# Optimization experiments

Hardware: AMD Instinct MI355X
Metric: run time of the kernel (lower is better)

Reference implementation:

```python
import jax, jax.numpy as jnp
import numpy as np

MAX_LEN = 2048  # config.max_len; T == MAX_LEN here
NEG_FILL = float(np.iinfo(np.int32).min)  # exact masked-fill constant from source


def sinusoidal_pe(max_len, d_feature):
    # sinusoidal_init(max_len=2*config.max_len, squeeze=True) from the source
    pe = np.zeros((max_len, d_feature), dtype=np.float32)
    position = np.arange(0, max_len)[:, np.newaxis]
    scale_factor = -np.log(10000.0 / 1.0) / (d_feature // 2 - 1)
    div_term = 1.0 * np.exp(np.arange(0, d_feature // 2) * scale_factor)
    pe[:, :d_feature // 2] = np.sin(position * div_term)
    pe[:, d_feature // 2:2 * (d_feature // 2)] = np.cos(position * div_term)
    return jnp.asarray(pe)


def rel_shift_causal(logits):
    # logits: [B, T, T] (square -> causal branch of relative_shift), batched version
    b, t1, t2 = logits.shape
    pad = jnp.zeros_like(logits[..., :1])
    x = jnp.concatenate((pad, logits), axis=-1)      # [B, T, T+1]
    x = jnp.reshape(x, (b, t2 + 1, t1))
    x = x[:, 1:, :]                                  # drop first row
    return jnp.reshape(x, (b, t1, t2))


def setup_inputs() -> dict:
    key = jax.random.key(0)
    ks = jax.random.split(key, 7)
    B, T, D = 8, 2048, 512
    s = 1.0 / np.sqrt(D)
    inputs = jax.random.normal(ks[0], (B, T, D), dtype=jnp.float32)
    Wq = jax.random.normal(ks[1], (D, D), dtype=jnp.float32) * s
    Wk = jax.random.normal(ks[2], (D, D), dtype=jnp.float32) * s
    Wv = jax.random.normal(ks[3], (D, D), dtype=jnp.float32) * s
    Wrel = jax.random.normal(ks[4], (D, D), dtype=jnp.float32) * s
    content_bias = jax.random.normal(ks[5], (D,), dtype=jnp.float32) * 0.02
    relative_bias = jax.random.normal(ks[6], (D,), dtype=jnp.float32) * 0.02
    # causal mask as built by nn.make_causal_mask: [B, 1, T, T]
    mask = jnp.tril(jnp.ones((T, T), dtype=bool))[None, None].repeat(B, axis=0)
    return {"inputs": inputs, "Wq": Wq, "Wk": Wk, "Wv": Wv, "Wrel": Wrel,
            "content_bias": content_bias, "relative_bias": relative_bias, "mask": mask}


def reference(inputs, Wq, Wk, Wv, Wrel, content_bias, relative_bias, mask):
    B, T, D = inputs.shape
    q = inputs @ Wq
    k = inputs @ Wk
    v = inputs @ Wv
    # content attention with learned content bias
    content_att = jnp.einsum('bqd,bkd->bqk', q + content_bias, k)
    # relative position attention (causal, idxs=None): pe slice [mid-T : mid]
    pe = sinusoidal_pe(2 * MAX_LEN, D)[MAX_LEN - T:MAX_LEN]  # [T, D]
    relative_key = pe @ Wrel                                  # Dense(no bias)
    relative_att = jnp.einsum('bqd,kd->bqk', q + relative_bias, relative_key)
    relative_att = rel_shift_causal(relative_att)
    attn = (content_att + relative_att) / jnp.sqrt(jnp.asarray(D, inputs.dtype))
    attn = jnp.where(mask.squeeze(1), attn, NEG_FILL)
    attn = jax.nn.softmax(attn, axis=-1)
    return attn @ v
```

## Files before the change

kernel.cpp:

```cpp
#include <hip/hip_runtime.h>

typedef __attribute__((ext_vector_type(8))) short short8;
typedef __attribute__((ext_vector_type(4))) float f32x4;
typedef __attribute__((ext_vector_type(4))) float fvec4;
typedef __attribute__((ext_vector_type(4))) unsigned short us4;

#define T_ 2048
#define D_ 512
#define SC_ 0.04419417382415922f

__device__ __forceinline__ unsigned short f2bf(float f) {
    unsigned int u = __float_as_uint(f);
    u += 0x7fffu + ((u >> 16) & 1u);
    return (unsigned short)(u >> 16);
}

__device__ __forceinline__ void gload16(const void* g, void* l) {
    __builtin_amdgcn_global_load_lds((const __attribute__((address_space(1))) unsigned int*)g,
                                     (__attribute__((address_space(3))) unsigned int*)l,
                                     16, 0, 0);
}

__global__ __launch_bounds__(256) void prep_all(
    const float* __restrict__ in_f,
    const float* __restrict__ Wq, const float* __restrict__ Wk,
    const float* __restrict__ Wv, const float* __restrict__ Wr,
    unsigned short* __restrict__ in_bf,
    unsigned short* __restrict__ WqT, unsigned short* __restrict__ WkT,
    unsigned short* __restrict__ WvT, unsigned short* __restrict__ WrT,
    unsigned short* __restrict__ pe)
{
    const int bb = blockIdx.x;
    const int tid = threadIdx.x;
    if (bb < 8192) {
        const int idx = bb * 256 + tid;
        fvec4 v = ((const fvec4*)in_f)[idx];
        us4 o;
        o.x = f2bf(v.x); o.y = f2bf(v.y); o.z = f2bf(v.z); o.w = f2bf(v.w);
        ((us4*)in_bf)[idx] = o;
    } else if (bb < 9216) {
        __shared__ float wt[32][33];
        const int t = bb - 8192;
        const int w = t >> 8, tile = t & 255;
        const int tr = (tile >> 4) * 32, tc = (tile & 15) * 32;
        const float* W = (w == 0) ? Wq : (w == 1) ? Wk : (w == 2) ? Wv : Wr;
        unsigned short* WT = (w == 0) ? WqT : (w == 1) ? WkT : (w == 2) ? WvT : WrT;
        const int r0 = tid >> 5, c0 = tid & 31;
#pragma unroll
        for (int p = 0; p < 4; ++p)
            wt[r0 + 8 * p][c0] = W[(long)(tr + r0 + 8 * p) * 512 + tc + c0];
        __syncthreads();
#pragma unroll
        for (int p = 0; p < 4; ++p)
            WT[(long)(tc + r0 + 8 * p) * 512 + tr + c0] = f2bf(wt[c0][r0 + 8 * p]);
    } else {
        const int idx = (bb - 9216) * 256 + tid;
        const int o = idx * 4;
        const int rpos = o >> 9;
        us4 ov;
#pragma unroll
        for (int e = 0; e < 4; ++e) {
            const int c = (o + e) & 511;
            const int ci = (c < 256) ? c : c - 256;
            const float dv = expf((float)ci * -0.03611898183128701f);
            const float ang = (float)rpos * dv;
            ((unsigned short*)&ov)[e] = f2bf((c < 256) ? sinf(ang) : cosf(ang));
        }
        ((us4*)pe)[idx] = ov;
    }
}

struct __align__(16) SMem {
    unsigned short At[128 * 64];
    unsigned short Bt[128 * 64];
};

__device__ __forceinline__ void gemm_core(const unsigned short* __restrict__ A, long lda,
                                          const unsigned short* __restrict__ B, long ldb,
                                          int kmax, SMem& sm, f32x4 (&acc)[4][4]) {
    const int tid = threadIdx.x;
    const int wid = tid >> 6;
    const int lane = tid & 63;
    const int quad = lane >> 4;
    const int lr = lane & 15;
    const int wm = (wid & 1) * 64;
    const int wn = (wid >> 1) * 64;
#pragma unroll
    for (int r = 0; r < 4; ++r)
#pragma unroll
        for (int c = 0; c < 4; ++c) acc[r][c] = (f32x4){0.f, 0.f, 0.f, 0.f};

    const int sr = tid >> 3;
    const int l8 = ((tid & 7) ^ (sr & 7)) * 8;
    const unsigned short* Ag = A + (long)sr * lda + l8;
    const unsigned short* Bg = B + (long)sr * ldb + l8;

    for (int kk = 0; kk < kmax; kk += 64) {
#pragma unroll
        for (int c = 0; c < 4; ++c) {
            gload16(Ag + (long)(32 * c) * lda + kk, &sm.At[c * 2048 + wid * 512]);
            gload16(Bg + (long)(32 * c) * ldb + kk, &sm.Bt[c * 2048 + wid * 512]);
        }
        __syncthreads();
#pragma unroll
        for (int ks = 0; ks < 2; ++ks) {
            short8 av[4], bv[4];
#pragma unroll
            for (int r = 0; r < 4; ++r) {
                const int row = wm + r * 16 + lr;
                av[r] = *(const short8*)&sm.At[row * 64 + (((ks * 4 + quad) ^ (row & 7)) * 8)];
            }
#pragma unroll
            for (int c = 0; c < 4; ++c) {
                const int row = wn + c * 16 + lr;
                bv[c] = *(const short8*)&sm.Bt[row * 64 + (((ks * 4 + quad) ^ (row & 7)) * 8)];
            }
#pragma unroll
            for (int r = 0; r < 4; ++r)
#pragma unroll
                for (int c = 0; c < 4; ++c)
                    acc[r][c] = __builtin_amdgcn_mfma_f32_16x16x32_bf16(av[r], bv[c], acc[r][c], 0, 0, 0);
        }
        __syncthreads();
    }
}

#define EPI_COORDS()                               \
    const int tid = threadIdx.x;                   \
    const int wid = tid >> 6;                      \
    const int lane = tid & 63;                     \
    const int quad = lane >> 4;                    \
    const int lr = lane & 15;                      \
    const int wm = (wid & 1) * 64;                 \
    const int wn = (wid >> 1) * 64;

__global__ __launch_bounds__(256, 3) void proj_kernel(
    const unsigned short* __restrict__ in_bf,
    const unsigned short* __restrict__ WqT, const unsigned short* __restrict__ WkT,
    const unsigned short* __restrict__ WvT, const unsigned short* __restrict__ WrT,
    const unsigned short* __restrict__ pe,
    const float* __restrict__ cb, const float* __restrict__ rb,
    unsigned short* __restrict__ qc, unsigned short* __restrict__ qr,
    unsigned short* __restrict__ kbf, unsigned short* __restrict__ vT,
    unsigned short* __restrict__ rk)
{
    __shared__ SMem sm;
    EPI_COORDS();
    const long TD = (long)T_ * D_;
    const long DT = (long)D_ * T_;
    f32x4 acc[4][4];
    const int t = blockIdx.x;
    if (t < 1024) {
        const int r = t & 511;
        const int it = r >> 2, jt = r & 3;
        const unsigned short* Bw = (t < 512) ? WqT : WkT;
        gemm_core(in_bf + (long)it * 128 * 512, 512, Bw + (long)jt * 128 * 512, 512, 512, sm, acc);
        const int i0 = it * 128, j0 = jt * 128;
#pragma unroll
        for (int r2 = 0; r2 < 4; ++r2)
#pragma unroll
            for (int c2 = 0; c2 < 4; ++c2) {
                const int gi = i0 + wm + r2 * 16 + quad * 4;
                const int gj = j0 + wn + c2 * 16 + lr;
#pragma unroll
                for (int tt = 0; tt < 4; ++tt) {
                    const float v = acc[r2][c2][tt];
                    const long row = gi + tt;
                    if (t < 512) {
                        qc[row * 512 + gj] = f2bf(v + cb[gj]);
                        qr[row * 512 + gj] = f2bf(v + rb[gj]);
                    } else {
                        kbf[row * 512 + gj] = f2bf(v);
                    }
                }
            }
    } else if (t < 1536) {
        const int r = t - 1024;
        const int z = r >> 6, rr = r & 63;
        const int it = rr >> 4, jt = rr & 15;
        const int i0 = it * 128, j0 = jt * 128;
        gemm_core(WvT + (long)i0 * 512, 512, in_bf + (long)z * TD + (long)j0 * 512, 512, 512, sm, acc);
#pragma unroll
        for (int r2 = 0; r2 < 4; ++r2)
#pragma unroll
            for (int c2 = 0; c2 < 4; ++c2) {
                const int gi = i0 + wm + r2 * 16 + quad * 4;
                const int gj = j0 + wn + c2 * 16 + lr;
#pragma unroll
                for (int tt = 0; tt < 4; ++tt)
                    vT[(long)z * DT + (long)(gi + tt) * 2048 + gj] = f2bf(acc[r2][c2][tt]);
            }
    } else {
        const int r = t - 1536;
        const int it = r >> 2, jt = r & 3;
        const int i0 = it * 128, j0 = jt * 128;
        gemm_core(pe + (long)i0 * 512, 512, WrT + (long)j0 * 512, 512, 512, sm, acc);
#pragma unroll
        for (int r2 = 0; r2 < 4; ++r2)
#pragma unroll
            for (int c2 = 0; c2 < 4; ++c2) {
                const int gi = i0 + wm + r2 * 16 + quad * 4;
                const int gj = j0 + wn + c2 * 16 + lr;
#pragma unroll
                for (int tt = 0; tt < 4; ++tt)
                    rk[(long)(gi + tt) * 512 + gj] = f2bf(acc[r2][c2][tt]);
            }
    }
}

__global__ __launch_bounds__(256, 3) void score_kernel(
    const unsigned short* __restrict__ qc, const unsigned short* __restrict__ qr,
    const unsigned short* __restrict__ kbf, const unsigned short* __restrict__ rk,
    float* __restrict__ C8, float* __restrict__ R8)
{
    __shared__ SMem sm;
    EPI_COORDS();
    const long TD = (long)T_ * D_;
    f32x4 acc[4][4];
    const int z = blockIdx.x & 7;
    const int rr = blockIdx.x >> 3;
    if (rr < 136) {
        const int r = rr;
        int a = (int)((sqrtf(8.f * (float)r + 1.f) - 1.f) * 0.5f);
        if ((a + 1) * (a + 2) / 2 <= r) ++a;
        if (a * (a + 1) / 2 > r) --a;
        const int b = r - a * (a + 1) / 2;
        const int i0 = a * 128, j0 = b * 128;
        gemm_core(qc + (long)z * TD + (long)i0 * 512, 512,
                  kbf + (long)z * TD + (long)j0 * 512, 512, 512, sm, acc);
        float* Cf = C8 + (long)z * 4194304L;
#pragma unroll
        for (int r2 = 0; r2 < 4; ++r2)
#pragma unroll
            for (int c2 = 0; c2 < 4; ++c2) {
                const int gi = i0 + wm + r2 * 16 + quad * 4;
                const int gj = j0 + wn + c2 * 16 + lr;
#pragma unroll
                for (int tt = 0; tt < 4; ++tt)
                    Cf[(long)(gi + tt) * 2048 + gj] = acc[r2][c2][tt] * SC_;
            }
    } else {
        const int r = rr - 136;
        int u = (int)((sqrtf(8.f * (float)r + 1.f) - 1.f) * 0.5f);
        if ((u + 1) * (u + 2) / 2 <= r) ++u;
        if (u * (u + 1) / 2 > r) --u;
        const int v2 = r - u * (u + 1) / 2;
        const int a = u, b = 15 - u + v2;
        const int i0 = a * 128, p0 = b * 128;
        gemm_core(qr + (long)z * TD + (long)i0 * 512, 512,
                  rk + (long)p0 * 512, 512, 512, sm, acc);
        float* Rf = R8 + (long)z * 4194304L;
#pragma unroll
        for (int r2 = 0; r2 < 4; ++r2)
#pragma unroll
            for (int c2 = 0; c2 < 4; ++c2) {
                const int gi = i0 + wm + r2 * 16 + quad * 4;
                const int gp = p0 + wn + c2 * 16 + lr;
#pragma unroll
                for (int tt = 0; tt < 4; ++tt)
                    Rf[(long)(gi + tt) * 2048 + gp] = acc[r2][c2][tt];
            }
    }
}

__global__ __launch_bounds__(256) void softmax_kernel(float* __restrict__ C8,
                                                      const float* __restrict__ R8) {
    float* Cm = C8 + (long)blockIdx.y * 4194304L;
    const float* Rm = R8 + (long)blockIdx.y * 4194304L;
    __shared__ float s[2048];
    __shared__ float red[8];
    const int tid = threadIdx.x;
    const int wid = tid >> 6;
    for (int ss = 0; ss < 8; ++ss) {
        const int i = blockIdx.x + 256 * ss;
        const int n = i + 1;
        float* crow = Cm + (long)i * 2048;
        const float* rrow = Rm + (long)i * 2048 + (2047 - i);
        __syncthreads();
        float lmax = -3.0e38f;
        for (int j = tid; j < n; j += 256) {
            float v = crow[j] + rrow[j] * SC_;
            s[j] = v; lmax = fmaxf(lmax, v);
        }
        for (int o = 32; o; o >>= 1) lmax = fmaxf(lmax, __shfl_down(lmax, o));
        if ((tid & 63) == 0) red[wid] = lmax;
        __syncthreads();
        if (tid == 0) red[4] = fmaxf(fmaxf(red[0], red[1]), fmaxf(red[2], red[3]));
        __syncthreads();
        const float m = red[4];
        float lsum = 0.f;
        for (int j = tid; j < n; j += 256) { float e = __expf(s[j] - m); s[j] = e; lsum += e; }
        for (int o = 32; o; o >>= 1) lsum += __shfl_down(lsum, o);
        __syncthreads();
        if ((tid & 63) == 0) red[wid] = lsum;
        __syncthreads();
        if (tid == 0) red[4] = 1.0f / (red[0] + red[1] + red[2] + red[3]);
        __syncthreads();
        const float inv = red[4];
        unsigned short* P = (unsigned short*)Cm;
        const int iend = ((i >> 7) + 1) << 7;
        for (int j = tid; j < iend; j += 256) {
            const float pv = (j < n) ? s[j] * inv : 0.f;
            P[(long)i * 4096 + j] = f2bf(pv);
        }
    }
}

__global__ __launch_bounds__(256, 3) void pv_kernel(
    const float* __restrict__ C8, const unsigned short* __restrict__ vT,
    float* __restrict__ out)
{
    __shared__ SMem sm;
    EPI_COORDS();
    const long TD = (long)T_ * D_;
    const long DT = (long)D_ * T_;
    f32x4 acc[4][4];
    const int z = blockIdx.x & 7;
    const int q = blockIdx.x >> 3;
    const int it = 15 - (q >> 2);
    const int jt = q & 3;
    const int i0 = it * 128, j0 = jt * 128;
    const int kmax = i0 + 128;
    gemm_core((const unsigned short*)(C8 + (long)z * 4194304L) + (long)i0 * 4096, 4096,
              vT + (long)z * DT + (long)j0 * 2048, 2048, kmax, sm, acc);
#pragma unroll
    for (int r2 = 0; r2 < 4; ++r2)
#pragma unroll
        for (int c2 = 0; c2 < 4; ++c2) {
            const int gi = i0 + wm + r2 * 16 + quad * 4;
            const int gj = j0 + wn + c2 * 16 + lr;
#pragma unroll
            for (int tt = 0; tt < 4; ++tt)
                out[(long)z * TD + (long)(gi + tt) * 512 + gj] = acc[r2][c2][tt];
        }
}

extern "C" void kernel_launch(void* const* d_in, const int* in_sizes, int n_in,
                              void* d_out, int out_size, void* d_ws, size_t ws_size,
                              hipStream_t stream) {
    (void)in_sizes; (void)n_in; (void)out_size; (void)ws_size;
    const float* inputs = (const float*)d_in[0];
    const float* Wq = (const float*)d_in[1];
    const float* Wk = (const float*)d_in[2];
    const float* Wv = (const float*)d_in[3];
    const float* Wrel = (const float*)d_in[4];
    const float* cb = (const float*)d_in[5];
    const float* rb = (const float*)d_in[6];
    float* out = (float*)d_out;

    char* ws = (char*)d_ws;
    unsigned short* in_bf = (unsigned short*)ws;
    unsigned short* WqT = (unsigned short*)(ws + 16777216);
    unsigned short* WkT = WqT + 262144;
    unsigned short* WvT = WkT + 262144;
    unsigned short* WrT = WvT + 262144;
    unsigned short* pe  = WrT + 262144;
    unsigned short* qc  = pe + 1048576;
    unsigned short* qr  = qc + 8388608;
    unsigned short* kbf = qr + 8388608;
    unsigned short* vT  = kbf + 8388608;
    unsigned short* rk  = vT + 8388608;
    float* C8 = (float*)(rk + 1048576);
    float* R8 = C8 + 33554432;

    prep_all<<<dim3(10240), 256, 0, stream>>>(inputs, Wq, Wk, Wv, Wrel,
                                              in_bf, WqT, WkT, WvT, WrT, pe);
    proj_kernel<<<dim3(1600), 256, 0, stream>>>(in_bf, WqT, WkT, WvT, WrT, pe, cb, rb,
                                                qc, qr, kbf, vT, rk);
    score_kernel<<<dim3(2176), 256, 0, stream>>>(qc, qr, kbf, rk, C8, R8);
    softmax_kernel<<<dim3(256, 8), 256, 0, stream>>>(C8, R8);
    pv_kernel<<<dim3(512), 256, 0, stream>>>(C8, vT, out);
}
```

Baseline: 375.9 us.

## Pre-shift and pre-scale relative scores in GEMM epilogue, vectorize softmax

```diff
diff --git a/kernel.cpp b/kernel.cpp
--- a/kernel.cpp
+++ b/kernel.cpp
@@ -257,52 +257,78 @@
                 const int gi = i0 + wm + r2 * 16 + quad * 4;
                 const int gp = p0 + wn + c2 * 16 + lr;
 #pragma unroll
-                for (int tt = 0; tt < 4; ++tt)
-                    Rf[(long)(gi + tt) * 2048 + gp] = acc[r2][c2][tt];
+                for (int tt = 0; tt < 4; ++tt) {
+                    const int row = gi + tt;
+                    const int j = gp + row - 2047;
+                    if (j >= 0)
+                        Rf[(long)row * 2048 + j] = acc[r2][c2][tt] * SC_;
+                }
             }
     }
 }
 
 __global__ __launch_bounds__(256) void softmax_kernel(float* __restrict__ C8,
                                                       const float* __restrict__ R8) {
+    const int i = blockIdx.x;
     float* Cm = C8 + (long)blockIdx.y * 4194304L;
     const float* Rm = R8 + (long)blockIdx.y * 4194304L;
     __shared__ float s[2048];
-    __shared__ float red[8];
+    __shared__ float red[5];
     const int tid = threadIdx.x;
     const int wid = tid >> 6;
-    for (int ss = 0; ss < 8; ++ss) {
-        const int i = blockIdx.x + 256 * ss;
-        const int n = i + 1;
-        float* crow = Cm + (long)i * 2048;
-        const float* rrow = Rm + (long)i * 2048 + (2047 - i);
-        __syncthreads();
-        float lmax = -3.0e38f;
-        for (int j = tid; j < n; j += 256) {
-            float v = crow[j] + rrow[j] * SC_;
-            s[j] = v; lmax = fmaxf(lmax, v);
-        }
-        for (int o = 32; o; o >>= 1) lmax = fmaxf(lmax, __shfl_down(lmax, o));
-        if ((tid & 63) == 0) red[wid] = lmax;
-        __syncthreads();
-        if (tid == 0) red[4] = fmaxf(fmaxf(red[0], red[1]), fmaxf(red[2], red[3]));
-        __syncthreads();
-        const float m = red[4];
-        float lsum = 0.f;
-        for (int j = tid; j < n; j += 256) { float e = __expf(s[j] - m); s[j] = e; lsum += e; }
-        for (int o = 32; o; o >>= 1) lsum += __shfl_down(lsum, o);
-        __syncthreads();
-        if ((tid & 63) == 0) red[wid] = lsum;
-        __syncthreads();
-        if (tid == 0) red[4] = 1.0f / (red[0] + red[1] + red[2] + red[3]);
-        __syncthreads();
-        const float inv = red[4];
-        unsigned short* P = (unsigned short*)Cm;
-        const int iend = ((i >> 7) + 1) << 7;
-        for (int j = tid; j < iend; j += 256) {
+    const int n = i + 1;
+    const int n4 = (n + 3) >> 2;
+    const f32x4* c4 = (const f32x4*)(Cm + (long)i * 2048);
+    const f32x4* r4 = (const f32x4*)(Rm + (long)i * 2048);
+    float lmax = -3.0e38f;
+    for (int j4 = tid; j4 < n4; j4 += 256) {
+        const f32x4 c = c4[j4];
+        const f32x4 r = r4[j4];
+        f32x4 v;
+#pragma unroll
+        for (int e = 0; e < 4; ++e) {
+            const int j = j4 * 4 + e;
+            const float vv = (j < n) ? c[e] + r[e] : -3.0e38f;
+            v[e] = vv;
+            lmax = fmaxf(lmax, vv);
+        }
+        *(f32x4*)&s[j4 * 4] = v;
+    }
+    for (int o = 32; o; o >>= 1) lmax = fmaxf(lmax, __shfl_down(lmax, o));
+    if ((tid & 63) == 0) red[wid] = lmax;
+    __syncthreads();
+    if (tid == 0) red[4] = fmaxf(fmaxf(red[0], red[1]), fmaxf(red[2], red[3]));
+    __syncthreads();
+    const float m = red[4];
+    float lsum = 0.f;
+    for (int j4 = tid; j4 < n4; j4 += 256) {
+        f32x4 v = *(f32x4*)&s[j4 * 4];
+#pragma unroll
+        for (int e = 0; e < 4; ++e) {
+            const float x = __expf(v[e] - m);
+            v[e] = x;
+            lsum += x;
+        }
+        *(f32x4*)&s[j4 * 4] = v;
+    }
+    for (int o = 32; o; o >>= 1) lsum += __shfl_down(lsum, o);
+    if ((tid & 63) == 0) red[wid] = lsum;
+    __syncthreads();
+    if (tid == 0) red[4] = 1.0f / (red[0] + red[1] + red[2] + red[3]);
+    __syncthreads();
+    const float inv = red[4];
+    unsigned short* P = (unsigned short*)Cm;
+    us4* Prow = (us4*)(P + (long)i * 4096);
+    const int iend4 = (((i >> 7) + 1) << 7) >> 2;
+    for (int j4 = tid; j4 < iend4; j4 += 256) {
+        us4 ov;
+#pragma unroll
+        for (int e = 0; e < 4; ++e) {
+            const int j = j4 * 4 + e;
             const float pv = (j < n) ? s[j] * inv : 0.f;
-            P[(long)i * 4096 + j] = f2bf(pv);
-        }
+            ov[e] = f2bf(pv);
+        }
+        Prow[j4] = ov;
     }
 }
 
@@ -368,6 +394,6 @@
     proj_kernel<<<dim3(1600), 256, 0, stream>>>(in_bf, WqT, WkT, WvT, WrT, pe, cb, rb,
                                                 qc, qr, kbf, vT, rk);
     score_kernel<<<dim3(2176), 256, 0, stream>>>(qc, qr, kbf, rk, C8, R8);
-    softmax_kernel<<<dim3(256, 8), 256, 0, stream>>>(C8, R8);
+    softmax_kernel<<<dim3(2048, 8), 256, 0, stream>>>(C8, R8);
     pv_kernel<<<dim3(512), 256, 0, stream>>>(C8, vT, out);
 }
```

After: 371.7 us. No clear change (-1.1%).
